# Optimization experiments

Measured on AMD Instinct MI355X. Metric: run time of the kernel, lower is better.

## Reference

```python
import jax, jax.numpy as jnp
import numpy as np

S, B, H = 512, 128, 1024

def setup_inputs() -> dict:
    key = jax.random.key(0)
    k1, k2, k3, k4 = jax.random.split(key, 4)
    return {
        "hidden": jax.random.normal(k1, (1, B, H), dtype=jnp.float32),
        "encoder_outputs": jax.random.normal(k2, (S, B, H), dtype=jnp.float32),
        "W_attn": jax.random.normal(k3, (H, H), dtype=jnp.float32) * (1.0 / np.sqrt(H)),
        "b_attn": jax.random.normal(k4, (H,), dtype=jnp.float32) * 0.01,
    }

def reference(hidden, encoder_outputs, W_attn, b_attn):
    # 'general' Luong attention: energy_i = h_dec . (W @ enc_i + b)
    # encoder_outputs: [S, B, H]; hidden: [1, B, H]
    energy = jnp.einsum('sbh,kh->sbk', encoder_outputs, W_attn) + b_attn  # [S,B,H]
    scores = jnp.einsum('bh,sbh->bs', hidden[0], energy)                   # [B,S]
    attn = jax.nn.softmax(scores, axis=1)
    return attn[:, None, :]  # [B,1,S]
```

## Files before the change

kernel.cpp:

```cpp
#include <hip/hip_runtime.h>

#define S 512
#define B 128
#define H 1024

__global__ __launch_bounds__(256) void calc_u_one(const float* __restrict__ hidden,
                                                  const float* __restrict__ W,
                                                  float* __restrict__ u) {
    const int t  = threadIdx.x;
    const int th = t & 15;
    const int kg = t >> 4;
    const int bg = blockIdx.x & 15;
    const int ht = blockIdx.x >> 4;
    const int b0 = bg * 8;
    const int h0 = ht * 64 + th * 4;

    __shared__ float hs[8][1028];
    __shared__ float red[16][8][64];

    const float4* __restrict__ hv = reinterpret_cast<const float4*>(hidden + (size_t)b0 * H);
#pragma unroll
    for (int i = 0; i < 8; ++i) {
        const float4 v = hv[i * 256 + t];
        *reinterpret_cast<float4*>(&hs[i][t * 4]) = v;
    }
    __syncthreads();

    float4 acc[8];
#pragma unroll
    for (int j = 0; j < 8; ++j) acc[j] = make_float4(0.f, 0.f, 0.f, 0.f);

#pragma unroll 4
    for (int kk = 0; kk < 64; ++kk) {
        const int k = kg * 64 + ((kk + kg * 8) & 63);
        const float4 w = *reinterpret_cast<const float4*>(W + (size_t)k * H + h0);
#pragma unroll
        for (int j = 0; j < 8; ++j) {
            const float hb = hs[j][k];
            acc[j].x = fmaf(hb, w.x, acc[j].x);
            acc[j].y = fmaf(hb, w.y, acc[j].y);
            acc[j].z = fmaf(hb, w.z, acc[j].z);
            acc[j].w = fmaf(hb, w.w, acc[j].w);
        }
    }

    __syncthreads();
#pragma unroll
    for (int j = 0; j < 8; ++j)
        *reinterpret_cast<float4*>(&red[kg][j][th * 4]) = acc[j];
    __syncthreads();

    if (t < 128) {
        const int b  = t >> 4;
        const int hq = (t & 15) * 4;
        float4 s = *reinterpret_cast<const float4*>(&red[0][b][hq]);
#pragma unroll
        for (int g = 1; g < 16; ++g) {
            const float4 v = *reinterpret_cast<const float4*>(&red[g][b][hq]);
            s.x += v.x; s.y += v.y; s.z += v.z; s.w += v.w;
        }
        *reinterpret_cast<float4*>(u + (size_t)(b0 + b) * H + ht * 64 + hq) = s;
    }
}

__global__ __launch_bounds__(256) void calc_scores(const float* __restrict__ enc,
                                                   const float* __restrict__ u,
                                                   float* __restrict__ scores) {
    const int wid  = threadIdx.x >> 6;
    const int lane = threadIdx.x & 63;
    const int w  = blockIdx.x * 4 + wid;
    const int b  = w & (B - 1);
    const int sg = w >> 7;
    const int s0 = sg * 8;

    const float4* __restrict__ u4 = reinterpret_cast<const float4*>(u + (size_t)b * H);
    const float4 uu0 = u4[lane];
    const float4 uu1 = u4[64 + lane];
    const float4 uu2 = u4[128 + lane];
    const float4 uu3 = u4[192 + lane];

    float acc[8];
#pragma unroll
    for (int j = 0; j < 8; ++j) {
        const float4* __restrict__ e4 =
            reinterpret_cast<const float4*>(enc + ((size_t)(s0 + j) * B + b) * H);
        const float4 e0 = e4[lane];
        const float4 e1 = e4[64 + lane];
        const float4 e2 = e4[128 + lane];
        const float4 e3 = e4[192 + lane];
        float a = e0.x * uu0.x + e0.y * uu0.y + e0.z * uu0.z + e0.w * uu0.w;
        a = fmaf(e1.x, uu1.x, a); a = fmaf(e1.y, uu1.y, a);
        a = fmaf(e1.z, uu1.z, a); a = fmaf(e1.w, uu1.w, a);
        a = fmaf(e2.x, uu2.x, a); a = fmaf(e2.y, uu2.y, a);
        a = fmaf(e2.z, uu2.z, a); a = fmaf(e2.w, uu2.w, a);
        a = fmaf(e3.x, uu3.x, a); a = fmaf(e3.y, uu3.y, a);
        a = fmaf(e3.z, uu3.z, a); a = fmaf(e3.w, uu3.w, a);
        acc[j] = a;
    }
#pragma unroll
    for (int j = 0; j < 8; ++j)
#pragma unroll
        for (int off = 32; off >= 1; off >>= 1)
            acc[j] += __shfl_xor(acc[j], off, 64);

    if (lane == 0) {
        float4* sp = reinterpret_cast<float4*>(scores + (size_t)b * S + s0);
        sp[0] = make_float4(acc[0], acc[1], acc[2], acc[3]);
        sp[1] = make_float4(acc[4], acc[5], acc[6], acc[7]);
    }
}

__global__ __launch_bounds__(256) void softmax_rows(const float* __restrict__ scores,
                                                    float* __restrict__ out) {
    const int b = blockIdx.x;
    const int t = threadIdx.x;
    const int wid = t >> 6, lane = t & 63;
    const float* __restrict__ row = scores + (size_t)b * S;
    float v0 = row[t];
    float v1 = row[t + 256];

    __shared__ float sm[4], ss[4];

    float m = fmaxf(v0, v1);
#pragma unroll
    for (int off = 32; off >= 1; off >>= 1)
        m = fmaxf(m, __shfl_xor(m, off, 64));
    if (lane == 0) sm[wid] = m;
    __syncthreads();
    m = fmaxf(fmaxf(sm[0], sm[1]), fmaxf(sm[2], sm[3]));

    float e0 = __expf(v0 - m);
    float e1 = __expf(v1 - m);
    float sum = e0 + e1;
#pragma unroll
    for (int off = 32; off >= 1; off >>= 1)
        sum += __shfl_xor(sum, off, 64);
    if (lane == 0) ss[wid] = sum;
    __syncthreads();
    sum = ss[0] + ss[1] + ss[2] + ss[3];

    const float inv = 1.f / sum;
    out[(size_t)b * S + t]       = e0 * inv;
    out[(size_t)b * S + t + 256] = e1 * inv;
}

extern "C" void kernel_launch(void* const* d_in, const int* in_sizes, int n_in,
                              void* d_out, int out_size, void* d_ws, size_t ws_size,
                              hipStream_t stream) {
    const float* hidden = (const float*)d_in[0];
    const float* enc    = (const float*)d_in[1];
    const float* W      = (const float*)d_in[2];

    float* u      = (float*)d_ws;
    float* scores = u + (size_t)B * H;
    float* out    = (float*)d_out;

    calc_u_one  <<<256,  256, 0, stream>>>(hidden, W, u);
    calc_scores <<<2048, 256, 0, stream>>>(enc, u, scores);
    softmax_rows<<<128,  256, 0, stream>>>(scores, out);
}
```

Before: 57.71 us.

## Remap calc_scores blocks to batch tiles and stage u in shared memory

```diff
diff --git a/kernel.cpp b/kernel.cpp
--- a/kernel.cpp
+++ b/kernel.cpp
@@ -66,47 +66,68 @@
 __global__ __launch_bounds__(256) void calc_scores(const float* __restrict__ enc,
                                                    const float* __restrict__ u,
                                                    float* __restrict__ scores) {
-    const int wid  = threadIdx.x >> 6;
-    const int lane = threadIdx.x & 63;
-    const int w  = blockIdx.x * 4 + wid;
-    const int b  = w & (B - 1);
-    const int sg = w >> 7;
-    const int s0 = sg * 8;
+    const int t    = threadIdx.x;
+    const int wid  = t >> 6;
+    const int lane = t & 63;
+    const int q  = blockIdx.x & 31;
+    const int so = blockIdx.x >> 5;
+    const int b0 = q * 4;
 
-    const float4* __restrict__ u4 = reinterpret_cast<const float4*>(u + (size_t)b * H);
-    const float4 uu0 = u4[lane];
-    const float4 uu1 = u4[64 + lane];
-    const float4 uu2 = u4[128 + lane];
-    const float4 uu3 = u4[192 + lane];
+    __shared__ float us[4 * 1024];
 
-    float acc[8];
+    const float4* __restrict__ uv = reinterpret_cast<const float4*>(u + (size_t)b0 * H);
 #pragma unroll
-    for (int j = 0; j < 8; ++j) {
-        const float4* __restrict__ e4 =
-            reinterpret_cast<const float4*>(enc + ((size_t)(s0 + j) * B + b) * H);
-        const float4 e0 = e4[lane];
-        const float4 e1 = e4[64 + lane];
-        const float4 e2 = e4[128 + lane];
-        const float4 e3 = e4[192 + lane];
-        float a = e0.x * uu0.x + e0.y * uu0.y + e0.z * uu0.z + e0.w * uu0.w;
-        a = fmaf(e1.x, uu1.x, a); a = fmaf(e1.y, uu1.y, a);
-        a = fmaf(e1.z, uu1.z, a); a = fmaf(e1.w, uu1.w, a);
-        a = fmaf(e2.x, uu2.x, a); a = fmaf(e2.y, uu2.y, a);
-        a = fmaf(e2.z, uu2.z, a); a = fmaf(e2.w, uu2.w, a);
-        a = fmaf(e3.x, uu3.x, a); a = fmaf(e3.y, uu3.y, a);
-        a = fmaf(e3.z, uu3.z, a); a = fmaf(e3.w, uu3.w, a);
-        acc[j] = a;
+    for (int i = 0; i < 4; ++i) {
+        const float4 v = uv[i * 256 + t];
+        *reinterpret_cast<float4*>(&us[(i * 256 + t) * 4]) = v;
     }
+    __syncthreads();
+
+    float acc[2][4];
 #pragma unroll
-    for (int j = 0; j < 8; ++j)
+    for (int js = 0; js < 2; ++js) {
+        const int s = so * 8 + wid * 2 + js;
 #pragma unroll
-        for (int off = 32; off >= 1; off >>= 1)
-            acc[j] += __shfl_xor(acc[j], off, 64);
+        for (int jb = 0; jb < 4; ++jb) {
+            const float4* __restrict__ e4 =
+                reinterpret_cast<const float4*>(enc + ((size_t)s * B + (b0 + jb)) * H);
+            const float4* __restrict__ u4 =
+                reinterpret_cast<const float4*>(&us[jb * 1024]);
+            const float4 e0 = e4[lane];
+            const float4 e1 = e4[64 + lane];
+            const float4 e2 = e4[128 + lane];
+            const float4 e3 = e4[192 + lane];
+            const float4 u0 = u4[lane];
+            const float4 u1 = u4[64 + lane];
+            const float4 u2 = u4[128 + lane];
+            const float4 u3 = u4[192 + lane];
+            float a = e0.x * u0.x + e0.y * u0.y + e0.z * u0.z + e0.w * u0.w;
+            a = fmaf(e1.x, u1.x, a); a = fmaf(e1.y, u1.y, a);
+            a = fmaf(e1.z, u1.z, a); a = fmaf(e1.w, u1.w, a);
+            a = fmaf(e2.x, u2.x, a); a = fmaf(e2.y, u2.y, a);
+            a = fmaf(e2.z, u2.z, a); a = fmaf(e2.w, u2.w, a);
+            a = fmaf(e3.x, u3.x, a); a = fmaf(e3.y, u3.y, a);
+            a = fmaf(e3.z, u3.z, a); a = fmaf(e3.w, u3.w, a);
+            acc[js][jb] = a;
+        }
+    }
+
+#pragma unroll
+    for (int js = 0; js < 2; ++js)
+#pragma unroll
+        for (int jb = 0; jb < 4; ++jb)
+#pragma unroll
+            for (int off = 32; off >= 1; off >>= 1)
+                acc[js][jb] += __shfl_xor(acc[js][jb], off, 64);
 
     if (lane == 0) {
-        float4* sp = reinterpret_cast<float4*>(scores + (size_t)b * S + s0);
-        sp[0] = make_float4(acc[0], acc[1], acc[2], acc[3]);
-        sp[1] = make_float4(acc[4], acc[5], acc[6], acc[7]);
+#pragma unroll
+        for (int js = 0; js < 2; ++js) {
+            const int s = so * 8 + wid * 2 + js;
+#pragma unroll
+            for (int jb = 0; jb < 4; ++jb)
+                scores[(size_t)(b0 + jb) * S + s] = acc[js][jb];
+        }
     }
 }
 
```

After: 58.43 us. About the same (+1.2%).
